# Performance work log

Hardware: AMD Instinct MI355X
Metric: run time of the kernel (lower is better)

Reference implementation:

```python
import jax, jax.numpy as jnp
import numpy as np

LOG_MAX = float(np.log(1000.0 / 16.0))  # dw/dh clamp from BoxCoder.decode
NMS_THRESH = 0.7


def setup_inputs() -> dict:
    key = jax.random.key(0)
    k1, k2, k3, k4, k5, k6 = jax.random.split(key, 6)
    N, B = 262144, 4
    im_h, im_w = 800, 1280
    # plausible anchors: random centers inside image, sizes in [16, 216]
    cx = jax.random.uniform(k1, (N,)) * im_w
    cy = jax.random.uniform(k2, (N,)) * im_h
    aw = jax.random.uniform(k3, (N,)) * 200.0 + 16.0
    ah = jax.random.uniform(k4, (N,)) * 200.0 + 16.0
    anchors = jnp.stack([cx - 0.5 * aw, cy - 0.5 * ah, cx + 0.5 * aw, cy + 0.5 * ah], axis=1).astype(jnp.float32)
    pred_bbox_deltas = (jax.random.normal(k5, (B, N, 4)) * 0.2).astype(jnp.float32)
    objectness = jax.random.normal(k6, (B, N)).astype(jnp.float32)
    return {
        'anchors': anchors,
        'pred_bbox_deltas': pred_bbox_deltas,
        'objectness': objectness,
        'im_h': im_h,
        'im_w': im_w,
        'post_nms_top_n': 1000,
    }


def _decode_clip(anchors, deltas, im_h, im_w):
    # BoxCoder.decode with weights (1,1,1,1), then clip to image bounds.
    aw = anchors[:, 2] - anchors[:, 0]          # [N]
    ah = anchors[:, 3] - anchors[:, 1]
    acx = anchors[:, 0] + 0.5 * aw
    acy = anchors[:, 1] + 0.5 * ah
    dx, dy = deltas[..., 0], deltas[..., 1]     # [B,N]
    dw = jnp.minimum(deltas[..., 2], LOG_MAX)
    dh = jnp.minimum(deltas[..., 3], LOG_MAX)
    pcx = dx * aw + acx
    pcy = dy * ah + acy
    pw = jnp.exp(dw) * aw
    ph = jnp.exp(dh) * ah
    x1 = jnp.clip(pcx - 0.5 * pw, 0.0, im_w)
    y1 = jnp.clip(pcy - 0.5 * ph, 0.0, im_h)
    x2 = jnp.clip(pcx + 0.5 * pw, 0.0, im_w)
    y2 = jnp.clip(pcy + 0.5 * ph, 0.0, im_h)
    return jnp.stack([x1, y1, x2, y2], axis=-1)  # [B,N,4]


def _nms_indices(boxes, scores, k):
    # Greedy NMS (torchvision semantics: suppress IoU > thresh), fixed k picks.
    bs = jax.lax.stop_gradient(boxes)           # indices are non-differentiable
    ss = jax.lax.stop_gradient(scores)
    areas = (bs[:, 2] - bs[:, 0]) * (bs[:, 3] - bs[:, 1])

    def body(cur, _):
        i = jnp.argmax(cur)
        picked = cur[i]
        bb = bs[i]
        ix1 = jnp.maximum(bb[0], bs[:, 0])
        iy1 = jnp.maximum(bb[1], bs[:, 1])
        ix2 = jnp.minimum(bb[2], bs[:, 2])
        iy2 = jnp.minimum(bb[3], bs[:, 3])
        inter = jnp.maximum(ix2 - ix1, 0.0) * jnp.maximum(iy2 - iy1, 0.0)
        barea = (bb[2] - bb[0]) * (bb[3] - bb[1])
        iou = inter / (barea + areas - inter + 1e-9)
        cur = jnp.where(iou > NMS_THRESH, -jnp.inf, cur).at[i].set(-jnp.inf)
        return cur, (i, picked)

    _, (idx, picked) = jax.lax.scan(body, ss, None, length=k)
    return idx, jnp.isfinite(picked)            # valid flags pad positions


def reference(anchors, pred_bbox_deltas, objectness, im_h, im_w, post_nms_top_n):
    boxes = _decode_clip(anchors, pred_bbox_deltas, float(im_h), float(im_w))  # [B,N,4]
    area = (boxes[..., 2] - boxes[..., 0]) * (boxes[..., 3] - boxes[..., 1])
    # area > 1 filter, expressed as score masking (keeps shapes static)
    scores = jnp.where(area > 1.0, objectness, -jnp.inf)

    idx, valid = jax.vmap(lambda b, s: _nms_indices(b, s, post_nms_top_n))(boxes, scores)
    kept_boxes = jnp.take_along_axis(boxes, idx[..., None], axis=1)   # [B,K,4]
    kept_scores = jnp.take_along_axis(scores, idx, axis=1)            # [B,K]
    vf = valid.astype(boxes.dtype)
    kept_boxes = kept_boxes * vf[..., None]
    kept_scores = jnp.where(valid, kept_scores, 0.0)
    # [B, K, 6] = (x1,y1,x2,y2,score,valid)
    return jnp.concatenate([kept_boxes, kept_scores[..., None], vf[..., None]], axis=-1)
```

## Files before the change

kernel.cpp:

```cpp
#include <hip/hip_runtime.h>
#include <cstdint>
#include <cstddef>

#define NBINS 32768
#define FINB 64u
#define CAP_C 2048
#define NW (CAP_C / 64)
#define WP (NW + 1)
#define TARGET 1792u
#define KMAX 1008
#define MROWS 16
#define HB 1024
#define HE 32768
#define CNT_STRIDE 64

typedef unsigned long long u64;

__device__ __forceinline__ unsigned orderable(float f) {
  unsigned b = __float_as_uint(f);
  return (b & 0x80000000u) ? ~b : (b | 0x80000000u);
}

__global__ void decode_kernel(const float4* __restrict__ anchors,
                              const float4* __restrict__ deltas,
                              const float* __restrict__ obj,
                              const int* __restrict__ im_h_p,
                              const int* __restrict__ im_w_p,
                              float4* __restrict__ boxes,
                              unsigned* __restrict__ keys,
                              unsigned* __restrict__ hist,
                              int N, int B) {
#pragma clang fp contract(off)
  int n = blockIdx.x * blockDim.x + threadIdx.x;
  int stride = gridDim.x * blockDim.x;
  for (int j = n; j < B * NBINS; j += stride) hist[j] = 0u;
  if (n >= N) return;
  float imw = (float)(*im_w_p);
  float imh = (float)(*im_h_p);
  float4 a = anchors[n];
  float aw = a.z - a.x;
  float ah = a.w - a.y;
  float acx = a.x + 0.5f * aw;
  float acy = a.y + 0.5f * ah;
  const float LOGM = 4.135166556742356f;
  for (int b = 0; b < B; ++b) {
    size_t off = (size_t)b * N + n;
    float4 d = deltas[off];
    float dw = fminf(d.z, LOGM), dh = fminf(d.w, LOGM);
    float pcx = d.x * aw + acx;
    float pcy = d.y * ah + acy;
    float pw = expf(dw) * aw;
    float ph = expf(dh) * ah;
    float x1 = fminf(fmaxf(pcx - 0.5f * pw, 0.0f), imw);
    float y1 = fminf(fmaxf(pcy - 0.5f * ph, 0.0f), imh);
    float x2 = fminf(fmaxf(pcx + 0.5f * pw, 0.0f), imw);
    float y2 = fminf(fmaxf(pcy + 0.5f * ph, 0.0f), imh);
    boxes[off] = make_float4(x1, y1, x2, y2);
    float area = (x2 - x1) * (y2 - y1);
    float sc = (area > 1.0f) ? obj[off] : -__builtin_inff();
    keys[off] = orderable(sc);
  }
}

__global__ void __launch_bounds__(HB) hist_kernel(const unsigned* __restrict__ keys,
                                                  unsigned* __restrict__ hist,
                                                  int N) {
  __shared__ unsigned hl[NBINS / 2];
  int t = threadIdx.x, b = blockIdx.y;
  for (int i = t; i < NBINS / 2; i += HB) hl[i] = 0u;
  __syncthreads();
  const uint4* kb = (const uint4*)(keys + (size_t)b * N) + (size_t)blockIdx.x * (HE / 4);
  int lim = HE / 4;
  int rem4 = (N - blockIdx.x * HE) / 4;
  if (lim > rem4) lim = rem4;
  for (int i = t; i < lim; i += HB) {
    uint4 v = kb[i];
    unsigned b0 = v.x >> 17, b1 = v.y >> 17, b2 = v.z >> 17, b3 = v.w >> 17;
    atomicAdd(&hl[b0 >> 1], (b0 & 1u) ? 65536u : 1u);
    atomicAdd(&hl[b1 >> 1], (b1 & 1u) ? 65536u : 1u);
    atomicAdd(&hl[b2 >> 1], (b2 & 1u) ? 65536u : 1u);
    atomicAdd(&hl[b3 >> 1], (b3 & 1u) ? 65536u : 1u);
  }
  __syncthreads();
  unsigned* hg = hist + (size_t)b * NBINS;
  for (int i = t; i < NBINS / 2; i += HB) {
    unsigned v = hl[i];
    unsigned clo = v & 0xFFFFu, chi = v >> 16;
    if (clo) atomicAdd(&hg[2 * i], clo);
    if (chi) atomicAdd(&hg[2 * i + 1], chi);
  }
}

__global__ void __launch_bounds__(1024) threshold_kernel(const unsigned* __restrict__ hist,
                                                         unsigned* __restrict__ T_lo) {
  const int BPT = NBINS / 1024;
  __shared__ unsigned s_part[1024];
  __shared__ unsigned s_T;
  int b = blockIdx.x, t = threadIdx.x;
  const unsigned* h = hist + (size_t)b * NBINS;
  if (t == 0) s_T = 0xFFFFFFFFu;
  unsigned mysum = 0;
  const uint4* h4 = (const uint4*)(h + t * BPT);
  for (int k = 0; k < BPT / 4; ++k) {
    int bin0 = t * BPT + k * 4;
    if (bin0 >= (int)FINB) {
      uint4 v = h4[k];
      mysum += v.x + v.y + v.z + v.w;
    }
  }
  s_part[t] = mysum;
  __syncthreads();
  for (int d = 1; d < 1024; d <<= 1) {
    unsigned v = (t + d < 1024) ? s_part[t + d] : 0u;
    __syncthreads();
    s_part[t] += v;
    __syncthreads();
  }
  unsigned total = s_part[0];
  unsigned target = (TARGET < total) ? TARGET : total;
  unsigned above = (t + 1 < 1024) ? s_part[t + 1] : 0u;
  if (total > 0u && above < target && s_part[t] >= target) {
    unsigned c = above;
    for (int k = BPT - 1; k >= 0; --k) {
      unsigned bin = (unsigned)(t * BPT + k);
      if (bin < FINB) break;
      unsigned hv = h[bin];
      c += hv;
      if (c >= target) {
        unsigned T = bin;
        if (c > CAP_C && (c - hv) > 0u) T = bin + 1u;
        s_T = T;
        break;
      }
    }
  }
  __syncthreads();
  if (t == 0) T_lo[b] = (total == 0u) ? 0xFFFFFFFFu : s_T;
}

__global__ void __launch_bounds__(1024) sort_kernel(const unsigned* __restrict__ keys,
                                                    const unsigned* __restrict__ T_lo,
                                                    const float4* __restrict__ boxes,
                                                    float4* __restrict__ sboxes,
                                                    float* __restrict__ sscore,
                                                    unsigned* __restrict__ cntw,
                                                    int N) {
  __shared__ u64 sk[CAP_C];
  __shared__ unsigned s_n;
  int b = blockIdx.x, t = threadIdx.x;
  if (t == 0) s_n = 0u;
  for (int i = t; i < CAP_C; i += 1024) sk[i] = 0ull;
  __syncthreads();
  unsigned T = T_lo[b];
  const uint4* k4 = (const uint4*)(keys + (size_t)b * N);
  for (int i = t; i < N / 4; i += 1024) {
    uint4 v = k4[i];
    int bi = i * 4;
    if ((v.x >> 17) >= T) { unsigned p = atomicAdd(&s_n, 1u); if (p < CAP_C) sk[p] = ((u64)v.x << 32) | (unsigned)(~(bi + 0)); }
    if ((v.y >> 17) >= T) { unsigned p = atomicAdd(&s_n, 1u); if (p < CAP_C) sk[p] = ((u64)v.y << 32) | (unsigned)(~(bi + 1)); }
    if ((v.z >> 17) >= T) { unsigned p = atomicAdd(&s_n, 1u); if (p < CAP_C) sk[p] = ((u64)v.z << 32) | (unsigned)(~(bi + 2)); }
    if ((v.w >> 17) >= T) { unsigned p = atomicAdd(&s_n, 1u); if (p < CAP_C) sk[p] = ((u64)v.w << 32) | (unsigned)(~(bi + 3)); }
  }
  __syncthreads();
  int cnt = (int)s_n;
  if (cnt > CAP_C) cnt = CAP_C;
  if (t == 0) cntw[b * CNT_STRIDE] = (unsigned)cnt;
  for (unsigned kk = 2; kk <= CAP_C; kk <<= 1) {
    for (unsigned j = kk >> 1; j >= 1u; j >>= 1) {
      if (j >= 64u) __syncthreads();
      unsigned pid = (unsigned)t;
      unsigned i = ((pid & ~(j - 1u)) << 1) | (pid & (j - 1u));
      unsigned p = i | j;
      u64 va = sk[i], vb = sk[p];
      bool up = ((i & kk) == 0u);
      bool sw = up ? (va < vb) : (va > vb);
      if (sw) { sk[i] = vb; sk[p] = va; }
    }
  }
  __syncthreads();
  for (int i = t; i < CAP_C; i += 1024) {
    u64 key = sk[i];
    float4 bx = make_float4(0.f, 0.f, 0.f, 0.f);
    float sc = -__builtin_inff();
    if (i < cnt) {
      unsigned idx = ~(unsigned)(key & 0xFFFFFFFFull);
      bx = boxes[(size_t)b * N + idx];
      unsigned u = (unsigned)(key >> 32);
      unsigned sb2 = (u & 0x80000000u) ? (u ^ 0x80000000u) : ~u;
      sc = __uint_as_float(sb2);
    }
    sboxes[(size_t)b * CAP_C + i] = bx;
    sscore[(size_t)b * CAP_C + i] = sc;
  }
}

__global__ void __launch_bounds__(256) mask_kernel(const float4* __restrict__ sboxes,
                                                   u64* __restrict__ mask) {
#pragma clang fp contract(off)
  __shared__ float4 sb[CAP_C];
  int b = blockIdx.y, t = threadIdx.x;
  int wave = t >> 6, lane = t & 63;
  const float4* src = sboxes + (size_t)b * CAP_C;
  for (int i = t; i < CAP_C; i += 256) sb[i] = src[i];
  __syncthreads();
  for (int r = 0; r < MROWS; ++r) {
    int row = blockIdx.x * MROWS + r;
    float4 rb = sb[row];
    float ra = (rb.z - rb.x) * (rb.w - rb.y);
    for (int chunk = wave; chunk < NW; chunk += 4) {
      float4 cb = sb[chunk * 64 + lane];
      float ix1 = fmaxf(rb.x, cb.x), iy1 = fmaxf(rb.y, cb.y);
      float ix2 = fminf(rb.z, cb.z), iy2 = fminf(rb.w, cb.w);
      float inter = fmaxf(ix2 - ix1, 0.0f) * fmaxf(iy2 - iy1, 0.0f);
      float ca = (cb.z - cb.x) * (cb.w - cb.y);
      float iou = inter / (ra + ca - inter + 1e-9f);
      u64 bal = __ballot(iou > 0.7f);
      if (lane == 0)
        mask[((size_t)b * CAP_C + row) * NW + chunk] = bal;
    }
  }
}

__global__ void __launch_bounds__(256, 1) walk_kernel(const u64* __restrict__ mask,
                                                      const float4* __restrict__ sboxes,
                                                      const float* __restrict__ sscore,
                                                      const unsigned* __restrict__ cntp,
                                                      float* __restrict__ out, int K) {
  __shared__ u64 s_buf[2][64 * WP];
  __shared__ int s_keep[KMAX];
  __shared__ int s_ctl[4];
  const int b = blockIdx.x;
  const int t = threadIdx.x;
  const int wave = t >> 6, lane = t & 63;
  const u64* M = mask + (size_t)b * CAP_C * NW;
  int cnt = (int)cntp[b * CNT_STRIDE];
  if (cnt > CAP_C) cnt = CAP_C;
  const u64 lane_above = (lane == 63) ? 0ull : (~0ull << (lane + 1));

  for (int k = 0; k < 8; ++k) {
    int e = k * 256 + t;
    s_buf[0][(e >> 5) * WP + (e & 31)] = M[e];
  }
  if (t == 0) { s_ctl[0] = 0; s_ctl[1] = 0; s_ctl[2] = 0; }
  __syncthreads();

  u64 removed = 0ull;
  int nk = 0;
  int base = 0;
  int cur = 0;

  for (int tt = 0; tt < CAP_C / 64; ++tt) {
    int par = tt & 1;
    if (wave != 0) {
      int nt = base + 64;
      if (nt > CAP_C - 64) nt = CAP_C - 64;
      const u64* src = M + (size_t)nt * NW;
      u64* dst = s_buf[cur ^ 1];
      int s = t - 64;
      for (int k = 0; k < 11; ++k) {
        int e = k * 192 + s;
        if (e < 64 * NW)
          dst[(e >> 5) * WP + (e & 31)] = src[e];
      }
    } else {
      const u64* buf = s_buf[cur];
      int tw = base >> 6;
      u64 D = buf[(size_t)lane * WP + tw];
      unsigned rlo = __builtin_amdgcn_readlane((unsigned)(removed & 0xFFFFFFFFull), tw);
      unsigned rhi = __builtin_amdgcn_readlane((unsigned)(removed >> 32), tw);
      u64 in_rm = ((u64)rhi << 32) | (u64)rlo;
      int rem = cnt - base;
      u64 valid = (rem >= 64) ? ~0ull : ((rem <= 0) ? 0ull : ((1ull << rem) - 1ull));
      u64 pend = (~in_rm) & valid;
      u64 keep = 0ull;
      while (pend != 0ull) {
        bool cond = ((pend >> lane) & 1ull) && ((D & pend & lane_above) != 0ull);
        u64 bal = __ballot((int)cond);
        if (bal == 0ull) { keep |= pend; break; }
        int f = __builtin_ctzll(bal);
        u64 beq = (2ull << f) - 1ull;
        keep |= pend & beq;
        unsigned dlo = __builtin_amdgcn_readlane((unsigned)(D & 0xFFFFFFFFull), f);
        unsigned dhi = __builtin_amdgcn_readlane((unsigned)(D >> 32), f);
        u64 rowf = ((u64)dhi << 32) | (u64)dlo;
        pend &= ~beq;
        pend &= ~rowf;
      }
      int cap = K - nk;
      int kc = __popcll(keep);
      if (kc > cap) {
        bool mine = ((keep >> lane) & 1ull) &&
                    (__popcll(keep & ((1ull << lane) - 1ull)) < cap);
        keep = __ballot((int)mine);
        kc = cap;
      }
      if ((keep >> lane) & 1ull)
        s_keep[nk + __popcll(keep & ((1ull << lane) - 1ull))] = base + lane;
      nk += kc;
      int lw = lane & 31;
      u64 ac0 = 0, ac1 = 0, ac2 = 0, ac3 = 0;
#pragma unroll
      for (int r = 0; r < 64; r += 4) {
        u64 m0 = buf[(size_t)(r + 0) * WP + lw];
        u64 m1 = buf[(size_t)(r + 1) * WP + lw];
        u64 m2 = buf[(size_t)(r + 2) * WP + lw];
        u64 m3 = buf[(size_t)(r + 3) * WP + lw];
        ac0 |= m0 & ((u64)0 - ((keep >> (r + 0)) & 1ull));
        ac1 |= m1 & ((u64)0 - ((keep >> (r + 1)) & 1ull));
        ac2 |= m2 & ((u64)0 - ((keep >> (r + 2)) & 1ull));
        ac3 |= m3 & ((u64)0 - ((keep >> (r + 3)) & 1ull));
      }
      removed |= (ac0 | ac1) | (ac2 | ac3);
      int stop = (base + 64 >= cnt) || (nk >= K);
      if (lane == 0) { s_ctl[par] = stop; s_ctl[2] = nk; }
    }
    __syncthreads();
    if (s_ctl[par]) break;
    base += 64;
    cur ^= 1;
  }
  __syncthreads();
  int nkf = s_ctl[2];
  for (int j = t; j < nkf; j += 256) {
    int i = s_keep[j];
    float4 bx = sboxes[(size_t)b * CAP_C + i];
    float sc = sscore[(size_t)b * CAP_C + i];
    float* row = out + ((size_t)b * K + j) * 6;
    row[0] = bx.x; row[1] = bx.y; row[2] = bx.z; row[3] = bx.w;
    row[4] = sc; row[5] = 1.0f;
  }
  for (int j = nkf + t; j < K; j += 256) {
    float* row = out + ((size_t)b * K + j) * 6;
    row[0] = 0.f; row[1] = 0.f; row[2] = 0.f; row[3] = 0.f;
    row[4] = 0.f; row[5] = 0.f;
  }
}

extern "C" void kernel_launch(void* const* d_in, const int* in_sizes, int n_in,
                              void* d_out, int out_size, void* d_ws, size_t ws_size,
                              hipStream_t stream) {
  const float4* anchors = (const float4*)d_in[0];
  const float4* deltas = (const float4*)d_in[1];
  const float* obj = (const float*)d_in[2];
  const int* imh = (const int*)d_in[3];
  const int* imw = (const int*)d_in[4];
  int N = in_sizes[0] / 4;
  int B = in_sizes[2] / N;
  int K = out_size / (B * 6);
  if (K > KMAX) K = KMAX;

  char* ws = (char*)d_ws;
  size_t off = 0;
  float4* boxes = (float4*)(ws + off);            off += (size_t)B * N * 16;
  float4* sboxes = (float4*)(ws + off);           off += (size_t)B * CAP_C * 16;
  u64* mask = (u64*)(ws + off);                   off += (size_t)B * CAP_C * NW * 8;
  unsigned* keys = (unsigned*)(ws + off);         off += (size_t)B * N * 4;
  unsigned* hist = (unsigned*)(ws + off);         off += (size_t)B * NBINS * 4;
  float* sscore = (float*)(ws + off);             off += (size_t)B * CAP_C * 4;
  unsigned* T_lo = (unsigned*)(ws + off);         off += (size_t)B * 4;
  off = (off + 255) & ~(size_t)255;
  unsigned* cnt = (unsigned*)(ws + off);          off += (size_t)B * CNT_STRIDE * 4;
  float* out = (float*)d_out;

  int nb = (N + 255) / 256;
  int P = (N + HE - 1) / HE;
  decode_kernel<<<nb, 256, 0, stream>>>(anchors, deltas, obj, imh, imw,
                                        boxes, keys, hist, N, B);
  hist_kernel<<<dim3(P, B), HB, 0, stream>>>(keys, hist, N);
  threshold_kernel<<<B, 1024, 0, stream>>>(hist, T_lo);
  sort_kernel<<<B, 1024, 0, stream>>>(keys, T_lo, boxes, sboxes, sscore, cnt, N);
  mask_kernel<<<dim3(CAP_C / MROWS, B), 256, 0, stream>>>(sboxes, mask);
  walk_kernel<<<B, 256, 0, stream>>>(mask, sboxes, sscore, cnt, out, K);
}
```

Baseline: 208.6 us.

## Split candidate compaction into a multi-block kernel ahead of the sort

Candidate selection over all N keys used to run inside the sort kernel on a single block per batch. It now runs in a separate compact_kernel with 64 blocks per batch, which gather candidates locally and reserve global slots with one atomic. The sort kernel only loads the compacted candidates. This spreads the serial 262K-key scan across many CUs. The cost is an extra launch and a global round trip of the candidate buffer, and candidate order now depends on which block wins each atomic (the sort keys still include the index, so the final order stays deterministic).

```diff
diff --git a/kernel.cpp b/kernel.cpp
--- a/kernel.cpp
+++ b/kernel.cpp
@@ -13,6 +13,7 @@
 #define HB 1024
 #define HE 32768
 #define CNT_STRIDE 64
+#define CPB 64
 
 typedef unsigned long long u64;
 
@@ -92,13 +93,14 @@
 }
 
 __global__ void __launch_bounds__(1024) threshold_kernel(const unsigned* __restrict__ hist,
-                                                         unsigned* __restrict__ T_lo) {
+                                                         unsigned* __restrict__ T_lo,
+                                                         unsigned* __restrict__ cnt) {
   const int BPT = NBINS / 1024;
   __shared__ unsigned s_part[1024];
   __shared__ unsigned s_T;
   int b = blockIdx.x, t = threadIdx.x;
   const unsigned* h = hist + (size_t)b * NBINS;
-  if (t == 0) s_T = 0xFFFFFFFFu;
+  if (t == 0) { s_T = 0xFFFFFFFFu; cnt[b * CNT_STRIDE] = 0u; }
   unsigned mysum = 0;
   const uint4* h4 = (const uint4*)(h + t * BPT);
   for (int k = 0; k < BPT / 4; ++k) {
@@ -138,33 +140,50 @@
   if (t == 0) T_lo[b] = (total == 0u) ? 0xFFFFFFFFu : s_T;
 }
 
-__global__ void __launch_bounds__(1024) sort_kernel(const unsigned* __restrict__ keys,
-                                                    const unsigned* __restrict__ T_lo,
+__global__ void __launch_bounds__(1024) compact_kernel(const unsigned* __restrict__ keys,
+                                                       const unsigned* __restrict__ T_lo,
+                                                       u64* __restrict__ cand,
+                                                       unsigned* __restrict__ cnt, int N) {
+  __shared__ u64 s_w[4096];
+  __shared__ unsigned s_n, s_base;
+  int b = blockIdx.y, t = threadIdx.x;
+  if (t == 0) s_n = 0u;
+  __syncthreads();
+  unsigned T = T_lo[b];
+  int slice4 = N / 4 / CPB;
+  const uint4* k4 = (const uint4*)(keys + (size_t)b * N) + (size_t)blockIdx.x * slice4;
+  for (int i = t; i < slice4; i += 1024) {
+    uint4 v = k4[i];
+    int bi = (blockIdx.x * slice4 + i) * 4;
+    if ((v.x >> 17) >= T) { unsigned p = atomicAdd(&s_n, 1u); if (p < 4096u) s_w[p] = ((u64)v.x << 32) | (unsigned)(~(bi + 0)); }
+    if ((v.y >> 17) >= T) { unsigned p = atomicAdd(&s_n, 1u); if (p < 4096u) s_w[p] = ((u64)v.y << 32) | (unsigned)(~(bi + 1)); }
+    if ((v.z >> 17) >= T) { unsigned p = atomicAdd(&s_n, 1u); if (p < 4096u) s_w[p] = ((u64)v.z << 32) | (unsigned)(~(bi + 2)); }
+    if ((v.w >> 17) >= T) { unsigned p = atomicAdd(&s_n, 1u); if (p < 4096u) s_w[p] = ((u64)v.w << 32) | (unsigned)(~(bi + 3)); }
+  }
+  __syncthreads();
+  unsigned n = s_n < 4096u ? s_n : 4096u;
+  if (t == 0) s_base = (n > 0u) ? atomicAdd(&cnt[b * CNT_STRIDE], n) : 0u;
+  __syncthreads();
+  unsigned gb = s_base;
+  for (unsigned j = t; j < n; j += 1024) {
+    unsigned p = gb + j;
+    if (p < CAP_C) cand[(size_t)b * CAP_C + p] = s_w[j];
+  }
+}
+
+__global__ void __launch_bounds__(1024) sort_kernel(const u64* __restrict__ cand,
+                                                    const unsigned* __restrict__ cntp,
                                                     const float4* __restrict__ boxes,
                                                     float4* __restrict__ sboxes,
                                                     float* __restrict__ sscore,
-                                                    unsigned* __restrict__ cntw,
                                                     int N) {
   __shared__ u64 sk[CAP_C];
-  __shared__ unsigned s_n;
   int b = blockIdx.x, t = threadIdx.x;
-  if (t == 0) s_n = 0u;
-  for (int i = t; i < CAP_C; i += 1024) sk[i] = 0ull;
-  __syncthreads();
-  unsigned T = T_lo[b];
-  const uint4* k4 = (const uint4*)(keys + (size_t)b * N);
-  for (int i = t; i < N / 4; i += 1024) {
-    uint4 v = k4[i];
-    int bi = i * 4;
-    if ((v.x >> 17) >= T) { unsigned p = atomicAdd(&s_n, 1u); if (p < CAP_C) sk[p] = ((u64)v.x << 32) | (unsigned)(~(bi + 0)); }
-    if ((v.y >> 17) >= T) { unsigned p = atomicAdd(&s_n, 1u); if (p < CAP_C) sk[p] = ((u64)v.y << 32) | (unsigned)(~(bi + 1)); }
-    if ((v.z >> 17) >= T) { unsigned p = atomicAdd(&s_n, 1u); if (p < CAP_C) sk[p] = ((u64)v.z << 32) | (unsigned)(~(bi + 2)); }
-    if ((v.w >> 17) >= T) { unsigned p = atomicAdd(&s_n, 1u); if (p < CAP_C) sk[p] = ((u64)v.w << 32) | (unsigned)(~(bi + 3)); }
-  }
-  __syncthreads();
-  int cnt = (int)s_n;
+  int cnt = (int)cntp[b * CNT_STRIDE];
   if (cnt > CAP_C) cnt = CAP_C;
-  if (t == 0) cntw[b * CNT_STRIDE] = (unsigned)cnt;
+  for (int i = t; i < CAP_C; i += 1024)
+    sk[i] = (i < cnt) ? cand[(size_t)b * CAP_C + i] : 0ull;
+  __syncthreads();
   for (unsigned kk = 2; kk <= CAP_C; kk <<= 1) {
     for (unsigned j = kk >> 1; j >= 1u; j >>= 1) {
       if (j >= 64u) __syncthreads();
@@ -353,6 +372,7 @@
   size_t off = 0;
   float4* boxes = (float4*)(ws + off);            off += (size_t)B * N * 16;
   float4* sboxes = (float4*)(ws + off);           off += (size_t)B * CAP_C * 16;
+  u64* cand = (u64*)(ws + off);                   off += (size_t)B * CAP_C * 8;
   u64* mask = (u64*)(ws + off);                   off += (size_t)B * CAP_C * NW * 8;
   unsigned* keys = (unsigned*)(ws + off);         off += (size_t)B * N * 4;
   unsigned* hist = (unsigned*)(ws + off);         off += (size_t)B * NBINS * 4;
@@ -367,8 +387,9 @@
   decode_kernel<<<nb, 256, 0, stream>>>(anchors, deltas, obj, imh, imw,
                                         boxes, keys, hist, N, B);
   hist_kernel<<<dim3(P, B), HB, 0, stream>>>(keys, hist, N);
-  threshold_kernel<<<B, 1024, 0, stream>>>(hist, T_lo);
-  sort_kernel<<<B, 1024, 0, stream>>>(keys, T_lo, boxes, sboxes, sscore, cnt, N);
+  threshold_kernel<<<B, 1024, 0, stream>>>(hist, T_lo, cnt);
+  compact_kernel<<<dim3(CPB, B), 1024, 0, stream>>>(keys, T_lo, cand, cnt, N);
+  sort_kernel<<<B, 1024, 0, stream>>>(cand, cnt, boxes, sboxes, sscore, N);
   mask_kernel<<<dim3(CAP_C / MROWS, B), 256, 0, stream>>>(sboxes, mask);
   walk_kernel<<<B, 256, 0, stream>>>(mask, sboxes, sscore, cnt, out, K);
 }
```

Result: faster. 173.2 us (-17.0%).
